# Optimization experiments

Hardware: AMD Instinct MI355X
Metric: run time of the kernel (lower is better)

## Reference

```python
import jax, jax.numpy as jnp
import numpy as np

# Model dims (match init_kwargs)
B, N, COORD, F0 = 16, 512, 3, 64
K = 8            # kernels per layer
F1, F2 = 128, 256  # conv filters
POOL = 2
FC = 512
EPS = 1e-9


def _pairwise(C):
    """Pairwise euclidean distances D [B,N,N] and direction cosines Cos [B,N,N] from coords C [B,N,3]."""
    dot = jnp.einsum('bic,bjc->bij', C, C)
    l2 = jnp.einsum('bic,bic->bi', C, C)
    d2 = l2[:, :, None] + l2[:, None, :] - 2.0 * dot
    D = jnp.sqrt(jnp.abs(d2) + EPS)
    nrm = jnp.sqrt(l2 + EPS)
    Cos = dot / (nrm[:, :, None] * nrm[:, None, :])
    return D, Cos


def _layer(V, D, Cos, gkw, gkb, acw, acb, gcw, gcb, bng, bnb):
    """GraphKernels -> AngularContribution -> GraphConv -> tanh -> batchnorm (eval)."""
    b, n, f = V.shape
    # GraphKernels: node-dependent learned Gaussian decay over pairwise distances
    u = jax.nn.softplus(V @ gkw + gkb)                # [B,N,K]
    uk = jnp.transpose(u, (0, 2, 1))[..., None]       # [B,K,N,1]
    A = jnp.exp(-(D[:, None] ** 2) * uk)              # [B,K,N,N]
    # AngularContribution: learned interpolation between isotropic and cosine-weighted kernel
    w = jax.nn.sigmoid(V @ acw + acb)                 # [B,N,K]
    wk = jnp.transpose(w, (0, 2, 1))[..., None]       # [B,K,N,1]
    A = A * (wk * Cos[:, None] + (1.0 - wk))          # [B,K,N,N]
    # GraphConv: per-kernel message passing then shared dense over [self || messages]
    M = jnp.einsum('bkij,bjf->bikf', A, V).reshape(b, n, -1)  # [B,N,K*F]
    H = jnp.concatenate([V, M], axis=-1) @ gcw + gcb           # [B,N,F_out]
    H = jnp.tanh(H)
    # batchnorm in eval mode (moving mean 0, var 1): affine only
    return bng * H + bnb


def _pool(V, C, p):
    """AverageSeqGraphPool: average consecutive (sequence-ordered) nodes with window/stride p."""
    b, n, f = V.shape
    return V.reshape(b, n // p, p, f).mean(2), C.reshape(b, n // p, p, -1).mean(2)


def setup_inputs() -> dict:
    key = jax.random.key(0)
    ks = jax.random.split(key, 12)
    def w(k, shape):
        return jax.random.normal(k, shape, jnp.float32) / np.sqrt(shape[0])
    flat_dim = (N // POOL // POOL) * F2
    return {
        'V': jax.random.normal(ks[0], (B, N, F0), jnp.float32),
        'C': jax.random.normal(ks[1], (B, N, COORD), jnp.float32) * 10.0,  # ~Angstrom-scale coords
        'gk_w0': w(ks[2], (F0, K)), 'gk_b0': jnp.zeros((K,), jnp.float32),
        'ac_w0': w(ks[3], (F0, K)), 'ac_b0': jnp.zeros((K,), jnp.float32),
        'gc_w0': w(ks[4], ((K + 1) * F0, F1)), 'gc_b0': jnp.zeros((F1,), jnp.float32),
        'bn_g0': jnp.ones((F1,), jnp.float32), 'bn_b0': jnp.zeros((F1,), jnp.float32),
        'gk_w1': w(ks[5], (F1, K)), 'gk_b1': jnp.zeros((K,), jnp.float32),
        'ac_w1': w(ks[6], (F1, K)), 'ac_b1': jnp.zeros((K,), jnp.float32),
        'gc_w1': w(ks[7], ((K + 1) * F1, F2)), 'gc_b1': jnp.zeros((F2,), jnp.float32),
        'bn_g1': jnp.ones((F2,), jnp.float32), 'bn_b1': jnp.zeros((F2,), jnp.float32),
        'fc_w': w(ks[8], (flat_dim, FC)), 'fc_b': jnp.zeros((FC,), jnp.float32),
    }


def reference(V, C, gk_w0, gk_b0, ac_w0, ac_b0, gc_w0, gc_b0, bn_g0, bn_b0,
              gk_w1, gk_b1, ac_w1, ac_b1, gc_w1, gc_b1, bn_g1, bn_b1, fc_w, fc_b):
    D, Cos = _pairwise(C)
    H = _layer(V, D, Cos, gk_w0, gk_b0, ac_w0, ac_b0, gc_w0, gc_b0, bn_g0, bn_b0)
    H, C1 = _pool(H, C, POOL)
    D, Cos = _pairwise(C1)
    H = _layer(H, D, Cos, gk_w1, gk_b1, ac_w1, ac_b1, gc_w1, gc_b1, bn_g1, bn_b1)
    H, _ = _pool(H, C1, POOL)
    Flat = H.reshape(H.shape[0], -1)  # [B, 128*256]
    return jax.nn.sigmoid(Flat @ fc_w + fc_b)  # [B, 512]
```

## Files before the change

### kernel.cpp

```cpp
#include <hip/hip_runtime.h>
#include <math.h>

#define KK 8
#define EPSF 1e-9f

typedef unsigned int   uint32;
typedef unsigned short u16;
typedef __attribute__((ext_vector_type(8))) short bf16x8;
typedef __attribute__((ext_vector_type(4))) float f32x4;

#define MFMA_16x16x32(a, b, c) __builtin_amdgcn_mfma_f32_16x16x32_bf16(a, b, c, 0, 0, 0)

typedef __attribute__((address_space(1))) const unsigned int glob_cu32;
typedef __attribute__((address_space(3))) unsigned int lds_u32;
__device__ __forceinline__ void g2l16(const void* gsrc, void* ldst) {
    __builtin_amdgcn_global_load_lds((glob_cu32*)gsrc, (lds_u32*)ldst, 16, 0, 0);
}

__device__ __forceinline__ int swz(int row, int o) {
    return (row << 6) + (((o) ^ (row & 7)) << 3);
}

__device__ __forceinline__ float softplusf(float x) {
    return x > 0.0f ? x + log1pf(expf(-x)) : log1pf(expf(x));
}
__device__ __forceinline__ float sigmoidf_(float x) {
    return 1.0f / (1.0f + expf(-x));
}
__device__ __forceinline__ u16 f2bf(float f) {
    union { float f; uint32 u; } v; v.f = f;
    uint32 u = v.u;
    return (u16)((u + 0x7FFFu + ((u >> 16) & 1u)) >> 16);
}

__global__ __launch_bounds__(256)
void prep_kernel(const float* __restrict__ V, const float* __restrict__ W0,
                 const float* __restrict__ W1, u16* __restrict__ VT0,
                 u16* __restrict__ Wt0, u16* __restrict__ Wt1,
                 u16* __restrict__ X0) {
    __shared__ float s[64][65];
    int blk = blockIdx.x, tid = threadIdx.x;
    if (blk < 128) {
        int b = blk >> 3, rt = blk & 7;
#pragma unroll
        for (int t = 0; t < 16; t++) {
            int idx = t * 256 + tid; int r = idx >> 6, c = idx & 63;
            s[r][c] = V[((size_t)b * 512 + rt * 64 + r) * 64 + c];
        }
        __syncthreads();
#pragma unroll
        for (int t = 0; t < 16; t++) {
            int idx = t * 256 + tid; int f = idx >> 6, j = idx & 63;
            VT0[((size_t)b * 64 + f) * 512 + rt * 64 + j] = f2bf(s[j][f]);
        }
    } else if (blk < 146) {
        int t0 = blk - 128; int rt = t0 >> 1, ct = t0 & 1;
#pragma unroll
        for (int t = 0; t < 16; t++) {
            int idx = t * 256 + tid; int r = idx >> 6, c = idx & 63;
            s[r][c] = W0[((size_t)rt * 64 + r) * 128 + ct * 64 + c];
        }
        __syncthreads();
#pragma unroll
        for (int t = 0; t < 16; t++) {
            int idx = t * 256 + tid; int f = idx >> 6, j = idx & 63;
            Wt0[((size_t)ct * 64 + f) * 576 + rt * 64 + j] = f2bf(s[j][f]);
        }
    } else if (blk < 218) {
        int t0 = blk - 146; int rt = t0 >> 2, ct = t0 & 3;
#pragma unroll
        for (int t = 0; t < 16; t++) {
            int idx = t * 256 + tid; int r = idx >> 6, c = idx & 63;
            s[r][c] = W1[((size_t)rt * 64 + r) * 256 + ct * 64 + c];
        }
        __syncthreads();
#pragma unroll
        for (int t = 0; t < 16; t++) {
            int idx = t * 256 + tid; int f = idx >> 6, j = idx & 63;
            Wt1[((size_t)ct * 64 + f) * 1152 + rt * 64 + j] = f2bf(s[j][f]);
        }
    } else {
        int t0 = blk - 218;
#pragma unroll
        for (int q = 0; q < 16; q++) {
            int e = t0 * 4096 + q * 256 + tid;
            int row = e >> 6, c = e & 63;
            X0[(size_t)row * 576 + c] = f2bf(V[e]);
        }
    }
}

__global__ __launch_bounds__(256)
void t_h0p_kernel(const float* __restrict__ H0p, u16* __restrict__ VT1) {
    __shared__ float s[64][65];
    int blk = blockIdx.x, tid = threadIdx.x;
    int b = blk >> 3, rt = (blk >> 1) & 3, ct = blk & 1;
#pragma unroll
    for (int t = 0; t < 16; t++) {
        int idx = t * 256 + tid; int r = idx >> 6, c = idx & 63;
        s[r][c] = H0p[((size_t)b * 256 + rt * 64 + r) * 128 + ct * 64 + c];
    }
    __syncthreads();
#pragma unroll
    for (int t = 0; t < 16; t++) {
        int idx = t * 256 + tid; int f = idx >> 6, j = idx & 63;
        VT1[((size_t)b * 128 + ct * 64 + f) * 256 + rt * 64 + j] = f2bf(s[j][f]);
    }
}

__global__ __launch_bounds__(256)
void msg0_mfma(const u16* __restrict__ VT0, const float* __restrict__ C,
               const float* __restrict__ V,
               const float* __restrict__ gw, const float* __restrict__ gb,
               const float* __restrict__ aw, const float* __restrict__ ab,
               u16* __restrict__ X0) {
    int b = blockIdx.x >> 5, i0 = (blockIdx.x & 31) * 16;
    int tid = threadIdx.x;
    int wv = tid >> 6, lane = tid & 63, quad = lane >> 4, l15 = lane & 15;

    __shared__ __align__(16) u16 s_vT[64 * 64];
    __shared__ __align__(16) u16 s_A[128 * 64];
    __shared__ __align__(16) float s_ci[16][4];
    __shared__ __align__(16) float s_u[16][KK];
    __shared__ __align__(16) float s_w[16][KK];

    {
        int t = tid & 127;
        int i = t >> 3, k = t & 7;
        const float4* xr = (const float4*)(V + ((size_t)b * 512 + i0 + i) * 64);
        const float* wm = (tid < 128) ? gw : aw;
        float s = 0.f;
#pragma unroll
        for (int f4 = 0; f4 < 16; f4++) {
            float4 x = xr[f4];
            s += x.x * wm[(f4 * 4 + 0) * 8 + k] + x.y * wm[(f4 * 4 + 1) * 8 + k]
               + x.z * wm[(f4 * 4 + 2) * 8 + k] + x.w * wm[(f4 * 4 + 3) * 8 + k];
        }
        if (tid < 128) s_u[i][k] = softplusf(s + gb[k]);
        else           s_w[i][k] = sigmoidf_(s + ab[k]);
    }
    if (tid < 16) {
        const float* cp = C + ((size_t)b * 512 + i0 + tid) * 3;
        float x = cp[0], y = cp[1], z = cp[2];
        s_ci[tid][0] = x; s_ci[tid][1] = y; s_ci[tid][2] = z;
        s_ci[tid][3] = x * x + y * y + z * z;
    }
    __syncthreads();

    f32x4 acc[2][4] = {};

    for (int j0 = 0; j0 < 512; j0 += 64) {
        const float* cp = C + ((size_t)b * 512 + j0 + lane) * 3;
        float cjx = cp[0], cjy = cp[1], cjz = cp[2];
        float l2j = cjx * cjx + cjy * cjy + cjz * cjz;
        __syncthreads();
#pragma unroll
        for (int p = 0; p < 2; p++) {
            int s = p * 256 + wv * 64 + lane;
            int f = s >> 3, op = s & 7;
            g2l16(VT0 + ((size_t)b * 64 + f) * 512 + j0 + ((op ^ (f & 7)) << 3),
                  (void*)(s_vT + (p * 256 + wv * 64) * 8));
        }
#pragma unroll
        for (int t = 0; t < 4; t++) {
            int i = t * 4 + wv, j = lane;
            float dot = s_ci[i][0] * cjx + s_ci[i][1] * cjy + s_ci[i][2] * cjz;
            float d2 = fabsf(s_ci[i][3] + l2j - 2.f * dot) + EPSF;
            float cs = dot / sqrtf((s_ci[i][3] + EPSF) * (l2j + EPSF));
            f32x4 u01 = *(const f32x4*)&s_u[i][0];
            f32x4 u23 = *(const f32x4*)&s_u[i][4];
            f32x4 w01 = *(const f32x4*)&s_w[i][0];
            f32x4 w23 = *(const f32x4*)&s_w[i][4];
#pragma unroll
            for (int k = 0; k < 4; k++) {
                float a = __expf(-d2 * u01[k]) * (w01[k] * cs + 1.f - w01[k]);
                int row = i * 8 + k;
                s_A[(row << 6) + (((j >> 3) ^ (row & 7)) << 3) + (j & 7)] = f2bf(a);
            }
#pragma unroll
            for (int k = 0; k < 4; k++) {
                float a = __expf(-d2 * u23[k]) * (w23[k] * cs + 1.f - w23[k]);
                int row = i * 8 + 4 + k;
                s_A[(row << 6) + (((j >> 3) ^ (row & 7)) << 3) + (j & 7)] = f2bf(a);
            }
        }
        __syncthreads();
#pragma unroll
        for (int ks = 0; ks < 2; ks++) {
            int o = ks * 4 + quad;
            bf16x8 a0 = *(const bf16x8*)&s_A[swz(wv * 32 + l15, o)];
            bf16x8 a1 = *(const bf16x8*)&s_A[swz(wv * 32 + 16 + l15, o)];
#pragma unroll
            for (int cf = 0; cf < 4; cf++) {
                bf16x8 bv = *(const bf16x8*)&s_vT[swz(cf * 16 + l15, o)];
                acc[0][cf] = MFMA_16x16x32(a0, bv, acc[0][cf]);
                acc[1][cf] = MFMA_16x16x32(a1, bv, acc[1][cf]);
            }
        }
    }
#pragma unroll
    for (int rf = 0; rf < 2; rf++)
#pragma unroll
        for (int cf = 0; cf < 4; cf++)
#pragma unroll
            for (int r = 0; r < 4; r++) {
                int arow = wv * 32 + rf * 16 + quad * 4 + r;
                int i = arow >> 3, k = arow & 7;
                X0[((size_t)b * 512 + i0 + i) * 576 + 64 + k * 64 + cf * 16 + l15] =
                    f2bf(acc[rf][cf][r]);
            }
}

__global__ __launch_bounds__(256)
void msg1_mfma(const u16* __restrict__ VT1, const float* __restrict__ C,
               const float* __restrict__ H0p,
               const float* __restrict__ gw, const float* __restrict__ gb,
               const float* __restrict__ aw, const float* __restrict__ ab,
               u16* __restrict__ X1) {
    int b = blockIdx.x >> 5, i0 = ((blockIdx.x >> 1) & 15) * 16, fh = blockIdx.x & 1;
    int tid = threadIdx.x;
    int wv = tid >> 6, lane = tid & 63, quad = lane >> 4, l15 = lane & 15;

    __shared__ __align__(16) u16 s_vT[64 * 64];
    __shared__ __align__(16) u16 s_A[128 * 64];
    __shared__ __align__(16) float s_ci[16][4];
    __shared__ __align__(16) float s_u[16][KK];
    __shared__ __align__(16) float s_w[16][KK];

    {
        int t = tid & 127;
        int i = t >> 3, k = t & 7;
        const float4* xr = (const float4*)(H0p + ((size_t)b * 256 + i0 + i) * 128);
        const float* wm = (tid < 128) ? gw : aw;
        float s = 0.f;
#pragma unroll
        for (int f4 = 0; f4 < 32; f4++) {
            float4 x = xr[f4];
            s += x.x * wm[(f4 * 4 + 0) * 8 + k] + x.y * wm[(f4 * 4 + 1) * 8 + k]
               + x.z * wm[(f4 * 4 + 2) * 8 + k] + x.w * wm[(f4 * 4 + 3) * 8 + k];
        }
        if (tid < 128) s_u[i][k] = softplusf(s + gb[k]);
        else           s_w[i][k] = sigmoidf_(s + ab[k]);
    }
    if (tid < 16) {
        const float* cp = C + ((size_t)b * 512 + 2 * (i0 + tid)) * 3;
        float x = 0.5f * (cp[0] + cp[3]);
        float y = 0.5f * (cp[1] + cp[4]);
        float z = 0.5f * (cp[2] + cp[5]);
        s_ci[tid][0] = x; s_ci[tid][1] = y; s_ci[tid][2] = z;
        s_ci[tid][3] = x * x + y * y + z * z;
    }
    __syncthreads();

    f32x4 acc[2][4] = {};

    for (int j0 = 0; j0 < 256; j0 += 64) {
        const float* cp = C + ((size_t)b * 512 + 2 * (j0 + lane)) * 3;
        float cjx = 0.5f * (cp[0] + cp[3]);
        float cjy = 0.5f * (cp[1] + cp[4]);
        float cjz = 0.5f * (cp[2] + cp[5]);
        float l2j = cjx * cjx + cjy * cjy + cjz * cjz;
        __syncthreads();
#pragma unroll
        for (int p = 0; p < 2; p++) {
            int s = p * 256 + wv * 64 + lane;
            int f = s >> 3, op = s & 7;
            g2l16(VT1 + ((size_t)b * 128 + fh * 64 + f) * 256 + j0 + ((op ^ (f & 7)) << 3),
                  (void*)(s_vT + (p * 256 + wv * 64) * 8));
        }
#pragma unroll
        for (int t = 0; t < 4; t++) {
            int i = t * 4 + wv, j = lane;
            float dot = s_ci[i][0] * cjx + s_ci[i][1] * cjy + s_ci[i][2] * cjz;
            float d2 = fabsf(s_ci[i][3] + l2j - 2.f * dot) + EPSF;
            float cs = dot / sqrtf((s_ci[i][3] + EPSF) * (l2j + EPSF));
            f32x4 u01 = *(const f32x4*)&s_u[i][0];
            f32x4 u23 = *(const f32x4*)&s_u[i][4];
            f32x4 w01 = *(const f32x4*)&s_w[i][0];
            f32x4 w23 = *(const f32x4*)&s_w[i][4];
#pragma unroll
            for (int k = 0; k < 4; k++) {
                float a = __expf(-d2 * u01[k]) * (w01[k] * cs + 1.f - w01[k]);
                int row = i * 8 + k;
                s_A[(row << 6) + (((j >> 3) ^ (row & 7)) << 3) + (j & 7)] = f2bf(a);
            }
#pragma unroll
            for (int k = 0; k < 4; k++) {
                float a = __expf(-d2 * u23[k]) * (w23[k] * cs + 1.f - w23[k]);
                int row = i * 8 + 4 + k;
                s_A[(row << 6) + (((j >> 3) ^ (row & 7)) << 3) + (j & 7)] = f2bf(a);
            }
        }
        __syncthreads();
#pragma unroll
        for (int ks = 0; ks < 2; ks++) {
            int o = ks * 4 + quad;
            bf16x8 a0 = *(const bf16x8*)&s_A[swz(wv * 32 + l15, o)];
            bf16x8 a1 = *(const bf16x8*)&s_A[swz(wv * 32 + 16 + l15, o)];
#pragma unroll
            for (int cf = 0; cf < 4; cf++) {
                bf16x8 bv = *(const bf16x8*)&s_vT[swz(cf * 16 + l15, o)];
                acc[0][cf] = MFMA_16x16x32(a0, bv, acc[0][cf]);
                acc[1][cf] = MFMA_16x16x32(a1, bv, acc[1][cf]);
            }
        }
    }
#pragma unroll
    for (int rf = 0; rf < 2; rf++)
#pragma unroll
        for (int cf = 0; cf < 4; cf++)
#pragma unroll
            for (int r = 0; r < 4; r++) {
                int arow = wv * 32 + rf * 16 + quad * 4 + r;
                int i = arow >> 3, k = arow & 7;
                X1[((size_t)b * 256 + i0 + i) * 1152 + 128 + k * 128 + fh * 64 + cf * 16 + l15] =
                    f2bf(acc[rf][cf][r]);
            }
}

__global__ __launch_bounds__(256)
void post0_mfma(const u16* __restrict__ X0, const u16* __restrict__ Wt,
                const float* __restrict__ bias, const float* __restrict__ bng,
                const float* __restrict__ bnb, float* __restrict__ H0p,
                u16* __restrict__ X1) {
    int row0 = (blockIdx.x >> 1) * 32, col0 = (blockIdx.x & 1) * 64;
    int tid = threadIdx.x;
    int wv = tid >> 6, lane = tid & 63, quad = lane >> 4, l15 = lane & 15;
    int rw = wv & 1, cw = wv >> 1;

    __shared__ __align__(16) u16 s_X[32 * 64];
    __shared__ __align__(16) u16 s_W[64 * 64];

    f32x4 acc[2] = {};

    for (int kc = 0; kc < 576; kc += 64) {
        __syncthreads();
        {
            int s = wv * 64 + lane;
            int r = s >> 3, op = s & 7;
            g2l16(X0 + ((size_t)row0 + r) * 576 + kc + ((op ^ (r & 7)) << 3),
                  (void*)(s_X + (wv * 64) * 8));
        }
#pragma unroll
        for (int p = 0; p < 2; p++) {
            int s = p * 256 + wv * 64 + lane;
            int c = s >> 3, op = s & 7;
            g2l16(Wt + ((size_t)col0 + c) * 576 + kc + ((op ^ (c & 7)) << 3),
                  (void*)(s_W + (p * 256 + wv * 64) * 8));
        }
        __syncthreads();
#pragma unroll
        for (int ks = 0; ks < 2; ks++) {
            int o = ks * 4 + quad;
            bf16x8 av = *(const bf16x8*)&s_X[swz(rw * 16 + l15, o)];
#pragma unroll
            for (int cf = 0; cf < 2; cf++) {
                bf16x8 bv = *(const bf16x8*)&s_W[swz(cw * 32 + cf * 16 + l15, o)];
                acc[cf] = MFMA_16x16x32(av, bv, acc[cf]);
            }
        }
    }
#pragma unroll
    for (int cf = 0; cf < 2; cf++) {
        int col = col0 + cw * 32 + cf * 16 + l15;
        float bs = bias[col], gg = bng[col], bb = bnb[col];
        float h0 = gg * tanhf(acc[cf][0] + bs) + bb;
        float h1 = gg * tanhf(acc[cf][1] + bs) + bb;
        float h2 = gg * tanhf(acc[cf][2] + bs) + bb;
        float h3 = gg * tanhf(acc[cf][3] + bs) + bb;
        float p0 = 0.5f * (h0 + h1), p1 = 0.5f * (h2 + h3);
        size_t pr = (size_t)(row0 >> 1) + rw * 8 + quad * 2;
        H0p[pr * 128 + col] = p0;
        H0p[(pr + 1) * 128 + col] = p1;
        X1[pr * 1152 + col] = f2bf(p0);
        X1[(pr + 1) * 1152 + col] = f2bf(p1);
    }
}

__global__ __launch_bounds__(256)
void post1_mfma(const u16* __restrict__ X1, const u16* __restrict__ Wt,
                const float* __restrict__ bias, const float* __restrict__ bng,
                const float* __restrict__ bnb, float* __restrict__ H1p) {
    int row0 = (blockIdx.x >> 2) * 32, col0 = (blockIdx.x & 3) * 64;
    int tid = threadIdx.x;
    int wv = tid >> 6, lane = tid & 63, quad = lane >> 4, l15 = lane & 15;
    int rw = wv & 1, cw = wv >> 1;

    __shared__ __align__(16) u16 s_X[32 * 64];
    __shared__ __align__(16) u16 s_W[64 * 64];

    f32x4 acc[2] = {};

    for (int kc = 0; kc < 1152; kc += 64) {
        __syncthreads();
        {
            int s = wv * 64 + lane;
            int r = s >> 3, op = s & 7;
            g2l16(X1 + ((size_t)row0 + r) * 1152 + kc + ((op ^ (r & 7)) << 3),
                  (void*)(s_X + (wv * 64) * 8));
        }
#pragma unroll
        for (int p = 0; p < 2; p++) {
            int s = p * 256 + wv * 64 + lane;
            int c = s >> 3, op = s & 7;
            g2l16(Wt + ((size_t)col0 + c) * 1152 + kc + ((op ^ (c & 7)) << 3),
                  (void*)(s_W + (p * 256 + wv * 64) * 8));
        }
        __syncthreads();
#pragma unroll
        for (int ks = 0; ks < 2; ks++) {
            int o = ks * 4 + quad;
            bf16x8 av = *(const bf16x8*)&s_X[swz(rw * 16 + l15, o)];
#pragma unroll
            for (int cf = 0; cf < 2; cf++) {
                bf16x8 bv = *(const bf16x8*)&s_W[swz(cw * 32 + cf * 16 + l15, o)];
                acc[cf] = MFMA_16x16x32(av, bv, acc[cf]);
            }
        }
    }
#pragma unroll
    for (int cf = 0; cf < 2; cf++) {
        int col = col0 + cw * 32 + cf * 16 + l15;
        float bs = bias[col], gg = bng[col], bb = bnb[col];
        float h0 = gg * tanhf(acc[cf][0] + bs) + bb;
        float h1 = gg * tanhf(acc[cf][1] + bs) + bb;
        float h2 = gg * tanhf(acc[cf][2] + bs) + bb;
        float h3 = gg * tanhf(acc[cf][3] + bs) + bb;
        float p0 = 0.5f * (h0 + h1), p1 = 0.5f * (h2 + h3);
        size_t pr = (size_t)(row0 >> 1) + rw * 8 + quad * 2;
        H1p[pr * 256 + col] = p0;
        H1p[(pr + 1) * 256 + col] = p1;
    }
}

__global__ __launch_bounds__(256)
void fc_partial_kernel(const float* __restrict__ Flat, const float* __restrict__ W,
                       float* __restrict__ P) {
    int cs = blockIdx.x & 3, ks = blockIdx.x >> 2;
    int m0 = ks * 256;
    int c4 = threadIdx.x & 31;
    int msub = threadIdx.x >> 5;

    __shared__ __align__(16) float xT[256][16];

#pragma unroll
    for (int q = 0; q < 16; q++) {
        int idx = q * 256 + threadIdx.x;
        int b = idx >> 8, mm = idx & 255;
        int bg = (b >> 2) ^ (mm & 3);
        xT[mm][(bg << 2) + (b & 3)] = Flat[(size_t)b * 32768 + m0 + mm];
    }
    __syncthreads();

    const float4* W4 = (const float4*)W;
    float4 acc[16] = {};

    for (int h = 0; h < 4; h++) {
        float4 wbuf[8];
#pragma unroll
        for (int i = 0; i < 8; i++) {
            int mm = msub * 32 + h * 8 + i;
            wbuf[i] = W4[(size_t)(m0 + mm) * 128 + cs * 32 + c4];
        }
#pragma unroll
        for (int i = 0; i < 8; i++) {
            int mm = msub * 32 + h * 8 + i;
#pragma unroll
            for (int bg = 0; bg < 4; bg++) {
                float4 xv = *(const float4*)&xT[mm][((bg ^ (mm & 3)) << 2)];
                acc[bg * 4 + 0].x += xv.x * wbuf[i].x; acc[bg * 4 + 0].y += xv.x * wbuf[i].y;
                acc[bg * 4 + 0].z += xv.x * wbuf[i].z; acc[bg * 4 + 0].w += xv.x * wbuf[i].w;
                acc[bg * 4 + 1].x += xv.y * wbuf[i].x; acc[bg * 4 + 1].y += xv.y * wbuf[i].y;
                acc[bg * 4 + 1].z += xv.y * wbuf[i].z; acc[bg * 4 + 1].w += xv.y * wbuf[i].w;
                acc[bg * 4 + 2].x += xv.z * wbuf[i].x; acc[bg * 4 + 2].y += xv.z * wbuf[i].y;
                acc[bg * 4 + 2].z += xv.z * wbuf[i].z; acc[bg * 4 + 2].w += xv.z * wbuf[i].w;
                acc[bg * 4 + 3].x += xv.w * wbuf[i].x; acc[bg * 4 + 3].y += xv.w * wbuf[i].y;
                acc[bg * 4 + 3].z += xv.w * wbuf[i].z; acc[bg * 4 + 3].w += xv.w * wbuf[i].w;
            }
        }
    }
    __syncthreads();
    __shared__ __align__(16) float red[8][32][4];
#pragma unroll
    for (int b = 0; b < 16; b++) {
        red[msub][c4][0] = acc[b].x; red[msub][c4][1] = acc[b].y;
        red[msub][c4][2] = acc[b].z; red[msub][c4][3] = acc[b].w;
        __syncthreads();
        if (msub == 0) {
            float4 s = make_float4(0.f, 0.f, 0.f, 0.f);
#pragma unroll
            for (int m = 0; m < 8; m++) {
                s.x += red[m][c4][0]; s.y += red[m][c4][1];
                s.z += red[m][c4][2]; s.w += red[m][c4][3];
            }
            *(float4*)&P[((size_t)ks * 16 + b) * 512 + cs * 128 + c4 * 4] = s;
        }
        __syncthreads();
    }
}

__global__ void fc_reduce_kernel(const float* __restrict__ P, const float* __restrict__ fcb,
                                 float* __restrict__ out) {
    int idx = blockIdx.x * 256 + threadIdx.x;
    float s0 = 0.f, s1 = 0.f;
#pragma unroll 8
    for (int ks = 0; ks < 128; ks += 2) {
        s0 += P[(size_t)ks * 8192 + idx];
        s1 += P[(size_t)(ks + 1) * 8192 + idx];
    }
    float s = s0 + s1 + fcb[idx & 511];
    out[idx] = 1.f / (1.f + expf(-s));
}

extern "C" void kernel_launch(void* const* d_in, const int* in_sizes, int n_in,
                              void* d_out, int out_size, void* d_ws, size_t ws_size,
                              hipStream_t stream) {
    const float* V     = (const float*)d_in[0];
    const float* C     = (const float*)d_in[1];
    const float* gk_w0 = (const float*)d_in[2];
    const float* gk_b0 = (const float*)d_in[3];
    const float* ac_w0 = (const float*)d_in[4];
    const float* ac_b0 = (const float*)d_in[5];
    const float* gc_w0 = (const float*)d_in[6];
    const float* gc_b0 = (const float*)d_in[7];
    const float* bn_g0 = (const float*)d_in[8];
    const float* bn_b0 = (const float*)d_in[9];
    const float* gk_w1 = (const float*)d_in[10];
    const float* gk_b1 = (const float*)d_in[11];
    const float* ac_w1 = (const float*)d_in[12];
    const float* ac_b1 = (const float*)d_in[13];
    const float* gc_w1 = (const float*)d_in[14];
    const float* gc_b1 = (const float*)d_in[15];
    const float* bn_g1 = (const float*)d_in[16];
    const float* bn_b1 = (const float*)d_in[17];
    const float* fc_w  = (const float*)d_in[18];
    const float* fc_b  = (const float*)d_in[19];
    float* out = (float*)d_out;

    float* H0p = (float*)d_ws;
    float* H1p = H0p + 524288;
    u16* X0  = (u16*)(H1p + 524288);
    u16* X1  = X0 + 4718592;
    u16* VT0 = X1 + 4718592;
    u16* Wt0 = VT0 + 524288;
    u16* Wt1 = Wt0 + 73728;
    u16* VT1 = VT0;
    float* P = (float*)X0;

    prep_kernel<<<346, 256, 0, stream>>>(V, gc_w0, gc_w1, VT0, Wt0, Wt1, X0);
    msg0_mfma<<<512, 256, 0, stream>>>(VT0, C, V, gk_w0, gk_b0, ac_w0, ac_b0, X0);
    post0_mfma<<<512, 256, 0, stream>>>(X0, Wt0, gc_b0, bn_g0, bn_b0, H0p, X1);
    t_h0p_kernel<<<128, 256, 0, stream>>>(H0p, VT1);
    msg1_mfma<<<512, 256, 0, stream>>>(VT1, C, H0p, gk_w1, gk_b1, ac_w1, ac_b1, X1);
    post1_mfma<<<512, 256, 0, stream>>>(X1, Wt1, gc_b1, bn_g1, bn_b1, H1p);
    fc_partial_kernel<<<512, 256, 0, stream>>>(H1p, fc_w, P);
    fc_reduce_kernel<<<32, 256, 0, stream>>>(P, fc_b, out);
}
```

Baseline: 224.3 us.

## Fuse message passing with dense projection per layer, keeping concat rows in LDS

```diff
diff --git a/kernel.cpp b/kernel.cpp
--- a/kernel.cpp
+++ b/kernel.cpp
@@ -36,8 +36,7 @@
 __global__ __launch_bounds__(256)
 void prep_kernel(const float* __restrict__ V, const float* __restrict__ W0,
                  const float* __restrict__ W1, u16* __restrict__ VT0,
-                 u16* __restrict__ Wt0, u16* __restrict__ Wt1,
-                 u16* __restrict__ X0) {
+                 u16* __restrict__ Wt0, u16* __restrict__ Wt1) {
     __shared__ float s[64][65];
     int blk = blockIdx.x, tid = threadIdx.x;
     if (blk < 128) {
@@ -66,7 +65,7 @@
             int idx = t * 256 + tid; int f = idx >> 6, j = idx & 63;
             Wt0[((size_t)ct * 64 + f) * 576 + rt * 64 + j] = f2bf(s[j][f]);
         }
-    } else if (blk < 218) {
+    } else {
         int t0 = blk - 146; int rt = t0 >> 2, ct = t0 & 3;
 #pragma unroll
         for (int t = 0; t < 16; t++) {
@@ -79,50 +78,31 @@
             int idx = t * 256 + tid; int f = idx >> 6, j = idx & 63;
             Wt1[((size_t)ct * 64 + f) * 1152 + rt * 64 + j] = f2bf(s[j][f]);
         }
-    } else {
-        int t0 = blk - 218;
-#pragma unroll
-        for (int q = 0; q < 16; q++) {
-            int e = t0 * 4096 + q * 256 + tid;
-            int row = e >> 6, c = e & 63;
-            X0[(size_t)row * 576 + c] = f2bf(V[e]);
-        }
     }
 }
 
 __global__ __launch_bounds__(256)
-void t_h0p_kernel(const float* __restrict__ H0p, u16* __restrict__ VT1) {
-    __shared__ float s[64][65];
-    int blk = blockIdx.x, tid = threadIdx.x;
-    int b = blk >> 3, rt = (blk >> 1) & 3, ct = blk & 1;
-#pragma unroll
-    for (int t = 0; t < 16; t++) {
-        int idx = t * 256 + tid; int r = idx >> 6, c = idx & 63;
-        s[r][c] = H0p[((size_t)b * 256 + rt * 64 + r) * 128 + ct * 64 + c];
-    }
-    __syncthreads();
-#pragma unroll
-    for (int t = 0; t < 16; t++) {
-        int idx = t * 256 + tid; int f = idx >> 6, j = idx & 63;
-        VT1[((size_t)b * 128 + ct * 64 + f) * 256 + rt * 64 + j] = f2bf(s[j][f]);
-    }
-}
-
-__global__ __launch_bounds__(256)
-void msg0_mfma(const u16* __restrict__ VT0, const float* __restrict__ C,
-               const float* __restrict__ V,
-               const float* __restrict__ gw, const float* __restrict__ gb,
-               const float* __restrict__ aw, const float* __restrict__ ab,
-               u16* __restrict__ X0) {
-    int b = blockIdx.x >> 5, i0 = (blockIdx.x & 31) * 16;
+void layer0_fused(const u16* __restrict__ VT0, const float* __restrict__ C,
+                  const float* __restrict__ V,
+                  const float* __restrict__ gw, const float* __restrict__ gb,
+                  const float* __restrict__ aw, const float* __restrict__ ab,
+                  const u16* __restrict__ Wt0, const float* __restrict__ bias,
+                  const float* __restrict__ bng, const float* __restrict__ bnb,
+                  float* __restrict__ H0p, u16* __restrict__ VT1) {
+    int b = blockIdx.x >> 5, tile = blockIdx.x & 31;
+    int i0 = tile * 16;
     int tid = threadIdx.x;
     int wv = tid >> 6, lane = tid & 63, quad = lane >> 4, l15 = lane & 15;
 
-    __shared__ __align__(16) u16 s_vT[64 * 64];
-    __shared__ __align__(16) u16 s_A[128 * 64];
+    __shared__ __align__(16) u16 s_mem[12288];
+    __shared__ __align__(16) u16 s_X[16 * 584];
     __shared__ __align__(16) float s_ci[16][4];
-    __shared__ __align__(16) float s_u[16][KK];
-    __shared__ __align__(16) float s_w[16][KK];
+    __shared__ float s_u[16][KK];
+    __shared__ float s_w[16][KK];
+
+    u16* s_vT = s_mem;
+    u16* s_A  = s_mem + 4096;
+    u16* s_W  = s_mem;
 
     {
         int t = tid & 127;
@@ -145,10 +125,14 @@
         s_ci[tid][0] = x; s_ci[tid][1] = y; s_ci[tid][2] = z;
         s_ci[tid][3] = x * x + y * y + z * z;
     }
-    __syncthreads();
+    {
+        int row = tid >> 4, f4 = tid & 15;
+        float4 x = *(const float4*)(V + ((size_t)b * 512 + i0 + row) * 64 + f4 * 4);
+        *(uint32*)&s_X[row * 584 + f4 * 4]     = (uint32)f2bf(x.x) | ((uint32)f2bf(x.y) << 16);
+        *(uint32*)&s_X[row * 584 + f4 * 4 + 2] = (uint32)f2bf(x.z) | ((uint32)f2bf(x.w) << 16);
+    }
 
     f32x4 acc[2][4] = {};
-
     for (int j0 = 0; j0 < 512; j0 += 64) {
         const float* cp = C + ((size_t)b * 512 + j0 + lane) * 3;
         float cjx = cp[0], cjy = cp[1], cjz = cp[2];
@@ -198,6 +182,7 @@
             }
         }
     }
+
 #pragma unroll
     for (int rf = 0; rf < 2; rf++)
 #pragma unroll
@@ -206,32 +191,77 @@
             for (int r = 0; r < 4; r++) {
                 int arow = wv * 32 + rf * 16 + quad * 4 + r;
                 int i = arow >> 3, k = arow & 7;
-                X0[((size_t)b * 512 + i0 + i) * 576 + 64 + k * 64 + cf * 16 + l15] =
-                    f2bf(acc[rf][cf][r]);
-            }
+                s_X[i * 584 + 64 + k * 64 + cf * 16 + l15] = f2bf(acc[rf][cf][r]);
+            }
+
+    f32x4 acc2[2] = {};
+    for (int kc = 0; kc < 576; kc += 64) {
+        __syncthreads();
+#pragma unroll
+        for (int p = 0; p < 4; p++) {
+            int s = p * 256 + wv * 64 + lane;
+            int c = s >> 3, op = s & 7;
+            g2l16(Wt0 + (size_t)c * 576 + kc + ((op ^ (c & 7)) << 3),
+                  (void*)(s_W + (p * 256 + wv * 64) * 8));
+        }
+        __syncthreads();
+#pragma unroll
+        for (int ks = 0; ks < 2; ks++) {
+            int o = ks * 4 + quad;
+            bf16x8 av = *(const bf16x8*)&s_X[l15 * 584 + kc + o * 8];
+#pragma unroll
+            for (int cf = 0; cf < 2; cf++) {
+                bf16x8 bv = *(const bf16x8*)&s_W[swz(wv * 32 + cf * 16 + l15, o)];
+                acc2[cf] = MFMA_16x16x32(av, bv, acc2[cf]);
+            }
+        }
+    }
+
+#pragma unroll
+    for (int cf = 0; cf < 2; cf++) {
+        int col = wv * 32 + cf * 16 + l15;
+        float bs = bias[col], gg = bng[col], bb = bnb[col];
+        float h0 = gg * tanhf(acc2[cf][0] + bs) + bb;
+        float h1 = gg * tanhf(acc2[cf][1] + bs) + bb;
+        float h2 = gg * tanhf(acc2[cf][2] + bs) + bb;
+        float h3 = gg * tanhf(acc2[cf][3] + bs) + bb;
+        float p0 = 0.5f * (h0 + h1), p1 = 0.5f * (h2 + h3);
+        int pl = tile * 8 + quad * 2;
+        H0p[((size_t)b * 256 + pl) * 128 + col] = p0;
+        H0p[((size_t)b * 256 + pl + 1) * 128 + col] = p1;
+        VT1[((size_t)b * 128 + col) * 256 + pl]     = f2bf(p0);
+        VT1[((size_t)b * 128 + col) * 256 + pl + 1] = f2bf(p1);
+    }
 }
 
 __global__ __launch_bounds__(256)
-void msg1_mfma(const u16* __restrict__ VT1, const float* __restrict__ C,
-               const float* __restrict__ H0p,
-               const float* __restrict__ gw, const float* __restrict__ gb,
-               const float* __restrict__ aw, const float* __restrict__ ab,
-               u16* __restrict__ X1) {
-    int b = blockIdx.x >> 5, i0 = ((blockIdx.x >> 1) & 15) * 16, fh = blockIdx.x & 1;
+void layer1_fused(const u16* __restrict__ VT1, const float* __restrict__ C,
+                  const float* __restrict__ H0p,
+                  const float* __restrict__ gw, const float* __restrict__ gb,
+                  const float* __restrict__ aw, const float* __restrict__ ab,
+                  const u16* __restrict__ Wt1, const float* __restrict__ bias,
+                  const float* __restrict__ bng, const float* __restrict__ bnb,
+                  float* __restrict__ H1p) {
+    int b = blockIdx.x >> 5, tile = blockIdx.x & 31;
+    int i0 = tile * 8;
     int tid = threadIdx.x;
     int wv = tid >> 6, lane = tid & 63, quad = lane >> 4, l15 = lane & 15;
 
-    __shared__ __align__(16) u16 s_vT[64 * 64];
-    __shared__ __align__(16) u16 s_A[128 * 64];
-    __shared__ __align__(16) float s_ci[16][4];
-    __shared__ __align__(16) float s_u[16][KK];
-    __shared__ __align__(16) float s_w[16][KK];
-
-    {
-        int t = tid & 127;
+    __shared__ __align__(16) u16 s_mem[16384];
+    __shared__ __align__(16) u16 s_X1[8 * 1160];
+    __shared__ __align__(16) float s_ci[8][4];
+    __shared__ float s_u[8][KK];
+    __shared__ float s_w[8][KK];
+
+    u16* s_vT = s_mem;
+    u16* s_A  = s_mem + 8192;
+    u16* s_W  = s_mem;
+
+    if (wv < 2) {
+        int t = tid & 63;
         int i = t >> 3, k = t & 7;
         const float4* xr = (const float4*)(H0p + ((size_t)b * 256 + i0 + i) * 128);
-        const float* wm = (tid < 128) ? gw : aw;
+        const float* wm = (wv == 0) ? gw : aw;
         float s = 0.f;
 #pragma unroll
         for (int f4 = 0; f4 < 32; f4++) {
@@ -239,10 +269,10 @@
             s += x.x * wm[(f4 * 4 + 0) * 8 + k] + x.y * wm[(f4 * 4 + 1) * 8 + k]
                + x.z * wm[(f4 * 4 + 2) * 8 + k] + x.w * wm[(f4 * 4 + 3) * 8 + k];
         }
-        if (tid < 128) s_u[i][k] = softplusf(s + gb[k]);
-        else           s_w[i][k] = sigmoidf_(s + ab[k]);
-    }
-    if (tid < 16) {
+        if (wv == 0) s_u[i][k] = softplusf(s + gb[k]);
+        else         s_w[i][k] = sigmoidf_(s + ab[k]);
+    }
+    if (tid < 8) {
         const float* cp = C + ((size_t)b * 512 + 2 * (i0 + tid)) * 3;
         float x = 0.5f * (cp[0] + cp[3]);
         float y = 0.5f * (cp[1] + cp[4]);
@@ -250,10 +280,14 @@
         s_ci[tid][0] = x; s_ci[tid][1] = y; s_ci[tid][2] = z;
         s_ci[tid][3] = x * x + y * y + z * z;
     }
-    __syncthreads();
-
-    f32x4 acc[2][4] = {};
-
+    {
+        int row = tid >> 5, f4 = tid & 31;
+        float4 x = *(const float4*)(H0p + ((size_t)b * 256 + i0 + row) * 128 + f4 * 4);
+        *(uint32*)&s_X1[row * 1160 + f4 * 4]     = (uint32)f2bf(x.x) | ((uint32)f2bf(x.y) << 16);
+        *(uint32*)&s_X1[row * 1160 + f4 * 4 + 2] = (uint32)f2bf(x.z) | ((uint32)f2bf(x.w) << 16);
+    }
+
+    f32x4 acc[8] = {};
     for (int j0 = 0; j0 < 256; j0 += 64) {
         const float* cp = C + ((size_t)b * 512 + 2 * (j0 + lane)) * 3;
         float cjx = 0.5f * (cp[0] + cp[3]);
@@ -262,14 +296,14 @@
         float l2j = cjx * cjx + cjy * cjy + cjz * cjz;
         __syncthreads();
 #pragma unroll
-        for (int p = 0; p < 2; p++) {
+        for (int p = 0; p < 4; p++) {
             int s = p * 256 + wv * 64 + lane;
             int f = s >> 3, op = s & 7;
-            g2l16(VT1 + ((size_t)b * 128 + fh * 64 + f) * 256 + j0 + ((op ^ (f & 7)) << 3),
+            g2l16(VT1 + ((size_t)b * 128 + f) * 256 + j0 + ((op ^ (f & 7)) << 3),
                   (void*)(s_vT + (p * 256 + wv * 64) * 8));
         }
 #pragma unroll
-        for (int t = 0; t < 4; t++) {
+        for (int t = 0; t < 2; t++) {
             int i = t * 4 + wv, j = lane;
             float dot = s_ci[i][0] * cjx + s_ci[i][1] * cjy + s_ci[i][2] * cjz;
             float d2 = fabsf(s_ci[i][3] + l2j - 2.f * dot) + EPSF;
@@ -295,141 +329,61 @@
 #pragma unroll
         for (int ks = 0; ks < 2; ks++) {
             int o = ks * 4 + quad;
-            bf16x8 a0 = *(const bf16x8*)&s_A[swz(wv * 32 + l15, o)];
-            bf16x8 a1 = *(const bf16x8*)&s_A[swz(wv * 32 + 16 + l15, o)];
-#pragma unroll
-            for (int cf = 0; cf < 4; cf++) {
+            bf16x8 a0 = *(const bf16x8*)&s_A[swz(wv * 16 + l15, o)];
+#pragma unroll
+            for (int cf = 0; cf < 8; cf++) {
                 bf16x8 bv = *(const bf16x8*)&s_vT[swz(cf * 16 + l15, o)];
-                acc[0][cf] = MFMA_16x16x32(a0, bv, acc[0][cf]);
-                acc[1][cf] = MFMA_16x16x32(a1, bv, acc[1][cf]);
-            }
-        }
-    }
-#pragma unroll
-    for (int rf = 0; rf < 2; rf++)
-#pragma unroll
-        for (int cf = 0; cf < 4; cf++)
-#pragma unroll
-            for (int r = 0; r < 4; r++) {
-                int arow = wv * 32 + rf * 16 + quad * 4 + r;
-                int i = arow >> 3, k = arow & 7;
-                X1[((size_t)b * 256 + i0 + i) * 1152 + 128 + k * 128 + fh * 64 + cf * 16 + l15] =
-                    f2bf(acc[rf][cf][r]);
-            }
-}
-
-__global__ __launch_bounds__(256)
-void post0_mfma(const u16* __restrict__ X0, const u16* __restrict__ Wt,
-                const float* __restrict__ bias, const float* __restrict__ bng,
-                const float* __restrict__ bnb, float* __restrict__ H0p,
-                u16* __restrict__ X1) {
-    int row0 = (blockIdx.x >> 1) * 32, col0 = (blockIdx.x & 1) * 64;
-    int tid = threadIdx.x;
-    int wv = tid >> 6, lane = tid & 63, quad = lane >> 4, l15 = lane & 15;
-    int rw = wv & 1, cw = wv >> 1;
-
-    __shared__ __align__(16) u16 s_X[32 * 64];
-    __shared__ __align__(16) u16 s_W[64 * 64];
-
-    f32x4 acc[2] = {};
-
-    for (int kc = 0; kc < 576; kc += 64) {
-        __syncthreads();
-        {
-            int s = wv * 64 + lane;
-            int r = s >> 3, op = s & 7;
-            g2l16(X0 + ((size_t)row0 + r) * 576 + kc + ((op ^ (r & 7)) << 3),
-                  (void*)(s_X + (wv * 64) * 8));
-        }
-#pragma unroll
-        for (int p = 0; p < 2; p++) {
+                acc[cf] = MFMA_16x16x32(a0, bv, acc[cf]);
+            }
+        }
+    }
+
+#pragma unroll
+    for (int cf = 0; cf < 8; cf++)
+#pragma unroll
+        for (int r = 0; r < 4; r++) {
+            int arow = wv * 16 + quad * 4 + r;
+            int i = arow >> 3, k = arow & 7;
+            s_X1[i * 1160 + 128 + k * 128 + cf * 16 + l15] = f2bf(acc[cf][r]);
+        }
+
+    f32x4 acc2[4] = {};
+    for (int kc = 0; kc < 1152; kc += 64) {
+        __syncthreads();
+#pragma unroll
+        for (int p = 0; p < 8; p++) {
             int s = p * 256 + wv * 64 + lane;
             int c = s >> 3, op = s & 7;
-            g2l16(Wt + ((size_t)col0 + c) * 576 + kc + ((op ^ (c & 7)) << 3),
+            g2l16(Wt1 + (size_t)c * 1152 + kc + ((op ^ (c & 7)) << 3),
                   (void*)(s_W + (p * 256 + wv * 64) * 8));
         }
         __syncthreads();
 #pragma unroll
         for (int ks = 0; ks < 2; ks++) {
             int o = ks * 4 + quad;
-            bf16x8 av = *(const bf16x8*)&s_X[swz(rw * 16 + l15, o)];
-#pragma unroll
-            for (int cf = 0; cf < 2; cf++) {
-                bf16x8 bv = *(const bf16x8*)&s_W[swz(cw * 32 + cf * 16 + l15, o)];
-                acc[cf] = MFMA_16x16x32(av, bv, acc[cf]);
-            }
-        }
-    }
-#pragma unroll
-    for (int cf = 0; cf < 2; cf++) {
-        int col = col0 + cw * 32 + cf * 16 + l15;
+            bf16x8 av = *(const bf16x8*)&s_X1[(l15 & 7) * 1160 + kc + o * 8];
+#pragma unroll
+            for (int cf = 0; cf < 4; cf++) {
+                bf16x8 bv = *(const bf16x8*)&s_W[swz(wv * 64 + cf * 16 + l15, o)];
+                acc2[cf] = MFMA_16x16x32(av, bv, acc2[cf]);
+            }
+        }
+    }
+
+#pragma unroll
+    for (int cf = 0; cf < 4; cf++) {
+        int col = wv * 64 + cf * 16 + l15;
         float bs = bias[col], gg = bng[col], bb = bnb[col];
-        float h0 = gg * tanhf(acc[cf][0] + bs) + bb;
-        float h1 = gg * tanhf(acc[cf][1] + bs) + bb;
-        float h2 = gg * tanhf(acc[cf][2] + bs) + bb;
-        float h3 = gg * tanhf(acc[cf][3] + bs) + bb;
-        float p0 = 0.5f * (h0 + h1), p1 = 0.5f * (h2 + h3);
-        size_t pr = (size_t)(row0 >> 1) + rw * 8 + quad * 2;
-        H0p[pr * 128 + col] = p0;
-        H0p[(pr + 1) * 128 + col] = p1;
-        X1[pr * 1152 + col] = f2bf(p0);
-        X1[(pr + 1) * 1152 + col] = f2bf(p1);
-    }
-}
-
-__global__ __launch_bounds__(256)
-void post1_mfma(const u16* __restrict__ X1, const u16* __restrict__ Wt,
-                const float* __restrict__ bias, const float* __restrict__ bng,
-                const float* __restrict__ bnb, float* __restrict__ H1p) {
-    int row0 = (blockIdx.x >> 2) * 32, col0 = (blockIdx.x & 3) * 64;
-    int tid = threadIdx.x;
-    int wv = tid >> 6, lane = tid & 63, quad = lane >> 4, l15 = lane & 15;
-    int rw = wv & 1, cw = wv >> 1;
-
-    __shared__ __align__(16) u16 s_X[32 * 64];
-    __shared__ __align__(16) u16 s_W[64 * 64];
-
-    f32x4 acc[2] = {};
-
-    for (int kc = 0; kc < 1152; kc += 64) {
-        __syncthreads();
-        {
-            int s = wv * 64 + lane;
-            int r = s >> 3, op = s & 7;
-            g2l16(X1 + ((size_t)row0 + r) * 1152 + kc + ((op ^ (r & 7)) << 3),
-                  (void*)(s_X + (wv * 64) * 8));
-        }
-#pragma unroll
-        for (int p = 0; p < 2; p++) {
-            int s = p * 256 + wv * 64 + lane;
-            int c = s >> 3, op = s & 7;
-            g2l16(Wt + ((size_t)col0 + c) * 1152 + kc + ((op ^ (c & 7)) << 3),
-                  (void*)(s_W + (p * 256 + wv * 64) * 8));
-        }
-        __syncthreads();
-#pragma unroll
-        for (int ks = 0; ks < 2; ks++) {
-            int o = ks * 4 + quad;
-            bf16x8 av = *(const bf16x8*)&s_X[swz(rw * 16 + l15, o)];
-#pragma unroll
-            for (int cf = 0; cf < 2; cf++) {
-                bf16x8 bv = *(const bf16x8*)&s_W[swz(cw * 32 + cf * 16 + l15, o)];
-                acc[cf] = MFMA_16x16x32(av, bv, acc[cf]);
-            }
-        }
-    }
-#pragma unroll
-    for (int cf = 0; cf < 2; cf++) {
-        int col = col0 + cw * 32 + cf * 16 + l15;
-        float bs = bias[col], gg = bng[col], bb = bnb[col];
-        float h0 = gg * tanhf(acc[cf][0] + bs) + bb;
-        float h1 = gg * tanhf(acc[cf][1] + bs) + bb;
-        float h2 = gg * tanhf(acc[cf][2] + bs) + bb;
-        float h3 = gg * tanhf(acc[cf][3] + bs) + bb;
-        float p0 = 0.5f * (h0 + h1), p1 = 0.5f * (h2 + h3);
-        size_t pr = (size_t)(row0 >> 1) + rw * 8 + quad * 2;
-        H1p[pr * 256 + col] = p0;
-        H1p[(pr + 1) * 256 + col] = p1;
+        float h0 = gg * tanhf(acc2[cf][0] + bs) + bb;
+        float h1 = gg * tanhf(acc2[cf][1] + bs) + bb;
+        float h2 = gg * tanhf(acc2[cf][2] + bs) + bb;
+        float h3 = gg * tanhf(acc2[cf][3] + bs) + bb;
+        if (quad < 2) {
+            float p0 = 0.5f * (h0 + h1), p1 = 0.5f * (h2 + h3);
+            int pl = tile * 4 + quad * 2;
+            H1p[((size_t)b * 128 + pl) * 256 + col] = p0;
+            H1p[((size_t)b * 128 + pl + 1) * 256 + col] = p1;
+        }
     }
 }
 
@@ -539,20 +493,17 @@
 
     float* H0p = (float*)d_ws;
     float* H1p = H0p + 524288;
-    u16* X0  = (u16*)(H1p + 524288);
-    u16* X1  = X0 + 4718592;
-    u16* VT0 = X1 + 4718592;
-    u16* Wt0 = VT0 + 524288;
+    float* P   = H1p + 524288;
+    u16* VT0 = (u16*)(P + 1048576);
+    u16* VT1 = VT0 + 524288;
+    u16* Wt0 = VT1 + 524288;
     u16* Wt1 = Wt0 + 73728;
-    u16* VT1 = VT0;
-    float* P = (float*)X0;
-
-    prep_kernel<<<346, 256, 0, stream>>>(V, gc_w0, gc_w1, VT0, Wt0, Wt1, X0);
-    msg0_mfma<<<512, 256, 0, stream>>>(VT0, C, V, gk_w0, gk_b0, ac_w0, ac_b0, X0);
-    post0_mfma<<<512, 256, 0, stream>>>(X0, Wt0, gc_b0, bn_g0, bn_b0, H0p, X1);
-    t_h0p_kernel<<<128, 256, 0, stream>>>(H0p, VT1);
-    msg1_mfma<<<512, 256, 0, stream>>>(VT1, C, H0p, gk_w1, gk_b1, ac_w1, ac_b1, X1);
-    post1_mfma<<<512, 256, 0, stream>>>(X1, Wt1, gc_b1, bn_g1, bn_b1, H1p);
+
+    prep_kernel<<<218, 256, 0, stream>>>(V, gc_w0, gc_w1, VT0, Wt0, Wt1);
+    layer0_fused<<<512, 256, 0, stream>>>(VT0, C, V, gk_w0, gk_b0, ac_w0, ac_b0,
+                                          Wt0, gc_b0, bn_g0, bn_b0, H0p, VT1);
+    layer1_fused<<<512, 256, 0, stream>>>(VT1, C, H0p, gk_w1, gk_b1, ac_w1, ac_b1,
+                                          Wt1, gc_b1, bn_g1, bn_b1, H1p);
     fc_partial_kernel<<<512, 256, 0, stream>>>(H1p, fc_w, P);
     fc_reduce_kernel<<<32, 256, 0, stream>>>(P, fc_b, out);
 }
```

New measurement: 215.3 us. 1.04x faster.
